# Kernel tuning notes

Hardware: AMD Instinct MI355X
Metric: run time of the kernel (lower is better)

The kernel has to match this reference:

```python
import jax, jax.numpy as jnp
import numpy as np

B, S, D_IN, D_OUT, N_EXPERTS = 8, 4096, 512, 512, 8


def setup_inputs() -> dict:
    key = jax.random.key(0)
    k1, k2, k3, k4 = jax.random.split(key, 4)
    x = jax.random.normal(k1, (B, S, D_IN), dtype=jnp.float32)
    partitions = jax.random.randint(k2, (B, S), 0, N_EXPERTS, dtype=jnp.int32)
    # per-branch nn.Linear weights: [n, out_features, in_features], kaiming-ish scale
    W = jax.random.normal(k3, (N_EXPERTS, D_OUT, D_IN), dtype=jnp.float32) * 0.03
    b = jax.random.normal(k4, (N_EXPERTS, D_OUT), dtype=jnp.float32) * 0.01
    return {"x": x, "partitions": partitions, "W": W, "b": b}


def reference(x, partitions, W, b):
    # Hard token partition -> per-branch linear -> scatter combine.
    # Equivalent math to dynamic_partition + branch Linear + dynamic_stitch:
    # out[t] = x[t] @ W[p[t]].T + b[p[t]]
    in_shape = x.shape
    xf = x.reshape(-1, in_shape[-1])          # [T, d_in]
    p = partitions.reshape(-1)                # [T]
    # Compute all-expert outputs, then select per-token expert (vectorized
    # replacement for the variable-size per-partition GEMM loop).
    y = jnp.einsum('td,eod->teo', xf, W) + b[None, :, :]   # [T, n, d_out]
    out = jnp.take_along_axis(y, p[:, None, None], axis=1)[:, 0, :]  # [T, d_out]
    return out.reshape(in_shape[:-1] + (W.shape[1],))
```

## Files before the change

### kernel.cpp

```cpp
#include <hip/hip_runtime.h>
#include <hip/hip_bf16.h>

#define N_EXPERTS 8
#define T_TOKENS 32768
#define D 512
#define TILE 128
#define BK 64
#define MAX_MTILES 264
#define SORT_CAP (MAX_MTILES * TILE)

typedef __bf16 bf16x8 __attribute__((ext_vector_type(8)));
typedef float  f32x4  __attribute__((ext_vector_type(4)));
typedef unsigned short u16x8 __attribute__((ext_vector_type(8)));

__device__ __forceinline__ unsigned short f2bf(float f) {
    unsigned int u = __float_as_uint(f);
    u += 0x7FFFu + ((u >> 16) & 1u);
    return (unsigned short)(u >> 16);
}

__device__ __forceinline__ void gl2lds16(const void* g, void* l) {
    __builtin_amdgcn_global_load_lds(
        (const __attribute__((address_space(1))) void*)g,
        (__attribute__((address_space(3))) void*)l, 16, 0, 0);
}

__global__ void hist_kernel(const int* __restrict__ p, int* __restrict__ counts) {
    __shared__ int h[N_EXPERTS];
    int tid = threadIdx.x;
    if (tid < N_EXPERTS) h[tid] = 0;
    __syncthreads();
    for (int t = blockIdx.x * blockDim.x + tid; t < T_TOKENS; t += gridDim.x * blockDim.x)
        atomicAdd(&h[p[t]], 1);
    __syncthreads();
    if (tid < N_EXPERTS) atomicAdd(&counts[tid], h[tid]);
}

__global__ void offsets_kernel(const int* __restrict__ counts, int* __restrict__ ps) {
    int acc = 0;
    for (int e = 0; e < N_EXPERTS; e++) {
        ps[e] = acc;
        acc += ((counts[e] + TILE - 1) / TILE) * TILE;
    }
    ps[N_EXPERTS] = acc;
}

__global__ void scatter_kernel(const int* __restrict__ p, const int* __restrict__ ps,
                               int* __restrict__ fill, int* __restrict__ sorted) {
    __shared__ int lcount[N_EXPERTS];
    __shared__ int lbase[N_EXPERTS];
    int tid = threadIdx.x;
    if (tid < N_EXPERTS) lcount[tid] = 0;
    __syncthreads();
    int t = blockIdx.x * blockDim.x + tid;
    int e = 0, lrank = 0;
    if (t < T_TOKENS) {
        e = p[t];
        lrank = atomicAdd(&lcount[e], 1);
    }
    __syncthreads();
    if (tid < N_EXPERTS)
        lbase[tid] = (lcount[tid] > 0) ? atomicAdd(&fill[tid], lcount[tid]) : 0;
    __syncthreads();
    if (t < T_TOKENS)
        sorted[ps[e] + lbase[e] + lrank] = t;
}

__global__ __launch_bounds__(256) void gather_convert_x(
        const float* __restrict__ x, const int* __restrict__ sorted,
        const int* __restrict__ ps, unsigned short* __restrict__ xs) {
    int row = blockIdx.x * 4 + (threadIdx.x >> 6);
    if (row >= ps[N_EXPERTS]) return;
    int lane = threadIdx.x & 63;
    int tok = sorted[row];
    u16x8 o;
    if (tok >= 0) {
        const float4* src = (const float4*)(x + (size_t)tok * D + lane * 8);
        float4 a = src[0], b = src[1];
        o[0] = f2bf(a.x); o[1] = f2bf(a.y); o[2] = f2bf(a.z); o[3] = f2bf(a.w);
        o[4] = f2bf(b.x); o[5] = f2bf(b.y); o[6] = f2bf(b.z); o[7] = f2bf(b.w);
    } else {
        o = (u16x8)0;
    }
    *(u16x8*)&xs[(size_t)row * D + lane * 8] = o;
}

__global__ __launch_bounds__(256) void convert_w(
        const float* __restrict__ W, unsigned short* __restrict__ Wb) {
    size_t i = (size_t)(blockIdx.x * 256 + threadIdx.x) * 8;
    const float4* s = (const float4*)(W + i);
    float4 a = s[0], b = s[1];
    u16x8 o;
    o[0] = f2bf(a.x); o[1] = f2bf(a.y); o[2] = f2bf(a.z); o[3] = f2bf(a.w);
    o[4] = f2bf(b.x); o[5] = f2bf(b.y); o[6] = f2bf(b.z); o[7] = f2bf(b.w);
    *(u16x8*)&Wb[i] = o;
}

__global__ __launch_bounds__(256) void moe_gemm_bf16(
        const unsigned short* __restrict__ xs, const unsigned short* __restrict__ Wb,
        const float* __restrict__ bias, const int* __restrict__ ps,
        const int* __restrict__ sorted, float* __restrict__ out) {
    __shared__ int s_idx[TILE];
    __shared__ unsigned short sA[TILE * BK];
    __shared__ unsigned short sB[TILE * BK];

    int bn = blockIdx.x, bm = blockIdx.y;
    int row0 = bm * TILE;
    int total = ps[N_EXPERTS];
    if (row0 >= total) return;
    int e = 0;
    while (row0 >= ps[e + 1]) e++;

    int tid = threadIdx.x;
    if (tid < TILE) s_idx[tid] = sorted[row0 + tid];

    int wave = tid >> 6, lane = tid & 63;
    int wm = (wave >> 1) * 64, wn = (wave & 1) * 64;
    int lrow = lane & 15, lq = lane >> 4;

    int srow = lane >> 3;
    int swz = (lane & 7) ^ srow;
    const unsigned short* gA = xs + (size_t)(row0 + wave * 32 + srow) * D + swz * 8;
    const unsigned short* gB = Wb + (size_t)e * D * D
                             + (size_t)(bn * TILE + wave * 32 + srow) * D + swz * 8;
    unsigned short* lA = sA + (wave * 32) * BK;
    unsigned short* lB = sB + (wave * 32) * BK;

    f32x4 acc[4][4];
#pragma unroll
    for (int i = 0; i < 4; i++)
#pragma unroll
        for (int j = 0; j < 4; j++)
            acc[i][j] = (f32x4){0.f, 0.f, 0.f, 0.f};

    for (int kk = 0; kk < D; kk += BK) {
        __syncthreads();
#pragma unroll
        for (int t = 0; t < 4; t++) {
            gl2lds16(gA + (size_t)(t * 8) * D + kk, lA + t * 8 * BK);
            gl2lds16(gB + (size_t)(t * 8) * D + kk, lB + t * 8 * BK);
        }
        __syncthreads();
#pragma unroll
        for (int ks = 0; ks < 2; ks++) {
            bf16x8 af[4], bfr[4];
#pragma unroll
            for (int i = 0; i < 4; i++) {
                int row = wm + 16 * i + lrow;
                int cb = (ks * 4 + lq) ^ (lrow & 7);
                af[i] = *(const bf16x8*)&sA[row * BK + cb * 8];
            }
#pragma unroll
            for (int j = 0; j < 4; j++) {
                int row = wn + 16 * j + lrow;
                int cb = (ks * 4 + lq) ^ (lrow & 7);
                bfr[j] = *(const bf16x8*)&sB[row * BK + cb * 8];
            }
#pragma unroll
            for (int i = 0; i < 4; i++)
#pragma unroll
                for (int j = 0; j < 4; j++)
                    acc[i][j] = __builtin_amdgcn_mfma_f32_16x16x32_bf16(
                        af[i], bfr[j], acc[i][j], 0, 0, 0);
        }
    }

#pragma unroll
    for (int j = 0; j < 4; j++) {
        int ng = bn * TILE + wn + 16 * j + lrow;
        float bv = bias[e * D + ng];
#pragma unroll
        for (int i = 0; i < 4; i++) {
#pragma unroll
            for (int r = 0; r < 4; r++) {
                int mrow = wm + 16 * i + lq * 4 + r;
                int tok = s_idx[mrow];
                if (tok >= 0)
                    out[(size_t)tok * D + ng] = acc[i][j][r] + bv;
            }
        }
    }
}

__global__ __launch_bounds__(256) void moe_gemm_f32(
        const float* __restrict__ x, const float* __restrict__ W,
        const float* __restrict__ bias, const int* __restrict__ ps,
        const int* __restrict__ sorted, float* __restrict__ out) {
    __shared__ int s_idx[TILE];
    __shared__ unsigned short sA[TILE][BK + 8];
    __shared__ unsigned short sB[TILE][BK + 8];

    int bm = blockIdx.x, bn = blockIdx.y;
    int row0 = bm * TILE;
    int total = ps[N_EXPERTS];
    if (row0 >= total) return;
    int e = 0;
    while (row0 >= ps[e + 1]) e++;

    int tid = threadIdx.x;
    if (tid < TILE) s_idx[tid] = sorted[row0 + tid];
    __syncthreads();

    const float* Wb = W + (size_t)e * D * D + (size_t)(bn * TILE) * D;

    f32x4 acc[4][4];
#pragma unroll
    for (int i = 0; i < 4; i++)
#pragma unroll
        for (int j = 0; j < 4; j++)
            acc[i][j] = (f32x4){0.f, 0.f, 0.f, 0.f};

    int wave = tid >> 6, lane = tid & 63;
    int wm = (wave >> 1) * 64, wn = (wave & 1) * 64;
    int lrow = lane & 15, lq = lane >> 4;

    for (int kk = 0; kk < D; kk += BK) {
#pragma unroll
        for (int i = 0; i < 8; i++) {
            int flat = tid + i * 256;
            int r = flat >> 4, c = (flat & 15) << 2;
            int tok = s_idx[r];
            float4 v = make_float4(0.f, 0.f, 0.f, 0.f);
            if (tok >= 0) v = *(const float4*)(x + (size_t)tok * D + kk + c);
            ushort4 w4;
            w4.x = f2bf(v.x); w4.y = f2bf(v.y); w4.z = f2bf(v.z); w4.w = f2bf(v.w);
            *(ushort4*)&sA[r][c] = w4;
        }
#pragma unroll
        for (int i = 0; i < 8; i++) {
            int flat = tid + i * 256;
            int r = flat >> 4, c = (flat & 15) << 2;
            float4 v = *(const float4*)(Wb + (size_t)r * D + kk + c);
            ushort4 w4;
            w4.x = f2bf(v.x); w4.y = f2bf(v.y); w4.z = f2bf(v.z); w4.w = f2bf(v.w);
            *(ushort4*)&sB[r][c] = w4;
        }
        __syncthreads();
#pragma unroll
        for (int ks = 0; ks < 2; ks++) {
            bf16x8 af[4], bfr[4];
#pragma unroll
            for (int i = 0; i < 4; i++)
                af[i] = *(const bf16x8*)&sA[wm + 16 * i + lrow][ks * 32 + lq * 8];
#pragma unroll
            for (int j = 0; j < 4; j++)
                bfr[j] = *(const bf16x8*)&sB[wn + 16 * j + lrow][ks * 32 + lq * 8];
#pragma unroll
            for (int i = 0; i < 4; i++)
#pragma unroll
                for (int j = 0; j < 4; j++)
                    acc[i][j] = __builtin_amdgcn_mfma_f32_16x16x32_bf16(
                        af[i], bfr[j], acc[i][j], 0, 0, 0);
        }
        __syncthreads();
    }

#pragma unroll
    for (int j = 0; j < 4; j++) {
        int ng = bn * TILE + wn + 16 * j + lrow;
        float bv = bias[e * D + ng];
#pragma unroll
        for (int i = 0; i < 4; i++) {
#pragma unroll
            for (int r = 0; r < 4; r++) {
                int mrow = wm + 16 * i + lq * 4 + r;
                int tok = s_idx[mrow];
                if (tok >= 0)
                    out[(size_t)tok * D + ng] = acc[i][j][r] + bv;
            }
        }
    }
}

extern "C" void kernel_launch(void* const* d_in, const int* in_sizes, int n_in,
                              void* d_out, int out_size, void* d_ws, size_t ws_size,
                              hipStream_t stream) {
    const float* x    = (const float*)d_in[0];
    const int*   part = (const int*)d_in[1];
    const float* W    = (const float*)d_in[2];
    const float* b    = (const float*)d_in[3];
    float* out = (float*)d_out;

    const size_t xs_elems = (size_t)SORT_CAP * D;
    const size_t wb_elems = (size_t)N_EXPERTS * D * D;
    const size_t fast_bytes = (xs_elems + wb_elems) * 2 + SORT_CAP * 4 + 32 * 4;

    if (ws_size >= fast_bytes) {
        unsigned short* xs = (unsigned short*)d_ws;
        unsigned short* Wb = xs + xs_elems;
        int* sorted = (int*)(Wb + wb_elems);
        int* counts = sorted + SORT_CAP;
        int* fill   = counts + N_EXPERTS;
        int* ps     = fill + N_EXPERTS;

        hipMemsetAsync(sorted, 0xFF, SORT_CAP * sizeof(int), stream);
        hipMemsetAsync(counts, 0, (2 * N_EXPERTS + N_EXPERTS + 1) * sizeof(int), stream);

        hist_kernel<<<64, 256, 0, stream>>>(part, counts);
        offsets_kernel<<<1, 1, 0, stream>>>(counts, ps);
        scatter_kernel<<<(T_TOKENS + 255) / 256, 256, 0, stream>>>(part, ps, fill, sorted);
        gather_convert_x<<<SORT_CAP / 4, 256, 0, stream>>>(x, sorted, ps, xs);
        convert_w<<<(int)(wb_elems / 8 / 256), 256, 0, stream>>>(W, Wb);

        dim3 grid(D / TILE, MAX_MTILES);
        moe_gemm_bf16<<<grid, 256, 0, stream>>>(xs, Wb, b, ps, sorted, out);
    } else {
        int* sorted = (int*)d_ws;
        int* counts = sorted + SORT_CAP;
        int* fill   = counts + N_EXPERTS;
        int* ps     = fill + N_EXPERTS;

        hipMemsetAsync(sorted, 0xFF, SORT_CAP * sizeof(int), stream);
        hipMemsetAsync(counts, 0, (2 * N_EXPERTS + N_EXPERTS + 1) * sizeof(int), stream);

        hist_kernel<<<64, 256, 0, stream>>>(part, counts);
        offsets_kernel<<<1, 1, 0, stream>>>(counts, ps);
        scatter_kernel<<<(T_TOKENS + 255) / 256, 256, 0, stream>>>(part, ps, fill, sorted);

        dim3 grid(MAX_MTILES, D / TILE);
        moe_gemm_f32<<<grid, 256, 0, stream>>>(x, W, b, ps, sorted, out);
    }
}
```

Measured before the change: 187.9 us.

## Fuse offset and convert kernels, load GEMM fragments directly from global memory

Drops the single-thread offsets kernel: scatter, convert and GEMM each recompute the padded expert prefix sums from the counts. The x-gather/convert and W-convert kernels are merged into one launch. The bf16 GEMM no longer stages tiles through LDS. Each wave loads its MFMA fragments from global memory into double-buffered registers, removing the barriers and LDS traffic but duplicating global and cache reads across waves. The prefetch on the last iteration also reads one step past the end of K.

```diff
diff --git a/kernel.cpp b/kernel.cpp
--- a/kernel.cpp
+++ b/kernel.cpp
@@ -5,9 +5,10 @@
 #define T_TOKENS 32768
 #define D 512
 #define TILE 128
-#define BK 64
 #define MAX_MTILES 264
 #define SORT_CAP (MAX_MTILES * TILE)
+#define GCX_BLOCKS (SORT_CAP / 4)
+#define WCV_BLOCKS ((N_EXPERTS * D * D) / (256 * 8))
 
 typedef __bf16 bf16x8 __attribute__((ext_vector_type(8)));
 typedef float  f32x4  __attribute__((ext_vector_type(4)));
@@ -19,11 +20,7 @@
     return (unsigned short)(u >> 16);
 }
 
-__device__ __forceinline__ void gl2lds16(const void* g, void* l) {
-    __builtin_amdgcn_global_load_lds(
-        (const __attribute__((address_space(1))) void*)g,
-        (__attribute__((address_space(3))) void*)l, 16, 0, 0);
-}
+__device__ __forceinline__ int pad_tile(int c) { return (c + TILE - 1) & ~(TILE - 1); }
 
 __global__ void hist_kernel(const int* __restrict__ p, int* __restrict__ counts) {
     __shared__ int h[N_EXPERTS];
@@ -36,16 +33,7 @@
     if (tid < N_EXPERTS) atomicAdd(&counts[tid], h[tid]);
 }
 
-__global__ void offsets_kernel(const int* __restrict__ counts, int* __restrict__ ps) {
-    int acc = 0;
-    for (int e = 0; e < N_EXPERTS; e++) {
-        ps[e] = acc;
-        acc += ((counts[e] + TILE - 1) / TILE) * TILE;
-    }
-    ps[N_EXPERTS] = acc;
-}
-
-__global__ void scatter_kernel(const int* __restrict__ p, const int* __restrict__ ps,
+__global__ void scatter_kernel(const int* __restrict__ p, const int* __restrict__ counts,
                                int* __restrict__ fill, int* __restrict__ sorted) {
     __shared__ int lcount[N_EXPERTS];
     __shared__ int lbase[N_EXPERTS];
@@ -62,69 +50,75 @@
     if (tid < N_EXPERTS)
         lbase[tid] = (lcount[tid] > 0) ? atomicAdd(&fill[tid], lcount[tid]) : 0;
     __syncthreads();
-    if (t < T_TOKENS)
-        sorted[ps[e] + lbase[e] + lrank] = t;
-}
-
-__global__ __launch_bounds__(256) void gather_convert_x(
-        const float* __restrict__ x, const int* __restrict__ sorted,
-        const int* __restrict__ ps, unsigned short* __restrict__ xs) {
-    int row = blockIdx.x * 4 + (threadIdx.x >> 6);
-    if (row >= ps[N_EXPERTS]) return;
-    int lane = threadIdx.x & 63;
-    int tok = sorted[row];
-    u16x8 o;
-    if (tok >= 0) {
-        const float4* src = (const float4*)(x + (size_t)tok * D + lane * 8);
-        float4 a = src[0], b = src[1];
+    if (t < T_TOKENS) {
+        int base = 0;
+#pragma unroll
+        for (int i = 0; i < N_EXPERTS; i++)
+            if (e > i) base += pad_tile(counts[i]);
+        sorted[base + lbase[e] + lrank] = t;
+    }
+}
+
+__global__ __launch_bounds__(256) void convert_kernel(
+        const float* __restrict__ x, const float* __restrict__ W,
+        const int* __restrict__ sorted, const int* __restrict__ counts,
+        unsigned short* __restrict__ xs, unsigned short* __restrict__ Wb) {
+    int bid = blockIdx.x;
+    if (bid < GCX_BLOCKS) {
+        int row = bid * 4 + (threadIdx.x >> 6);
+        int total = 0;
+#pragma unroll
+        for (int i = 0; i < N_EXPERTS; i++) total += pad_tile(counts[i]);
+        if (row >= total) return;
+        int lane = threadIdx.x & 63;
+        int tok = sorted[row];
+        u16x8 o;
+        if (tok >= 0) {
+            const float4* src = (const float4*)(x + (size_t)tok * D + lane * 8);
+            float4 a = src[0], b = src[1];
+            o[0] = f2bf(a.x); o[1] = f2bf(a.y); o[2] = f2bf(a.z); o[3] = f2bf(a.w);
+            o[4] = f2bf(b.x); o[5] = f2bf(b.y); o[6] = f2bf(b.z); o[7] = f2bf(b.w);
+        } else {
+            o = (u16x8)0;
+        }
+        *(u16x8*)&xs[(size_t)row * D + lane * 8] = o;
+    } else {
+        size_t i = ((size_t)(bid - GCX_BLOCKS) * 256 + threadIdx.x) * 8;
+        const float4* s = (const float4*)(W + i);
+        float4 a = s[0], b = s[1];
+        u16x8 o;
         o[0] = f2bf(a.x); o[1] = f2bf(a.y); o[2] = f2bf(a.z); o[3] = f2bf(a.w);
         o[4] = f2bf(b.x); o[5] = f2bf(b.y); o[6] = f2bf(b.z); o[7] = f2bf(b.w);
-    } else {
-        o = (u16x8)0;
-    }
-    *(u16x8*)&xs[(size_t)row * D + lane * 8] = o;
-}
-
-__global__ __launch_bounds__(256) void convert_w(
-        const float* __restrict__ W, unsigned short* __restrict__ Wb) {
-    size_t i = (size_t)(blockIdx.x * 256 + threadIdx.x) * 8;
-    const float4* s = (const float4*)(W + i);
-    float4 a = s[0], b = s[1];
-    u16x8 o;
-    o[0] = f2bf(a.x); o[1] = f2bf(a.y); o[2] = f2bf(a.z); o[3] = f2bf(a.w);
-    o[4] = f2bf(b.x); o[5] = f2bf(b.y); o[6] = f2bf(b.z); o[7] = f2bf(b.w);
-    *(u16x8*)&Wb[i] = o;
-}
-
-__global__ __launch_bounds__(256) void moe_gemm_bf16(
+        *(u16x8*)&Wb[i] = o;
+    }
+}
+
+__global__ __launch_bounds__(256) void moe_gemm_direct(
         const unsigned short* __restrict__ xs, const unsigned short* __restrict__ Wb,
-        const float* __restrict__ bias, const int* __restrict__ ps,
+        const float* __restrict__ bias, const int* __restrict__ counts,
         const int* __restrict__ sorted, float* __restrict__ out) {
     __shared__ int s_idx[TILE];
-    __shared__ unsigned short sA[TILE * BK];
-    __shared__ unsigned short sB[TILE * BK];
-
     int bn = blockIdx.x, bm = blockIdx.y;
     int row0 = bm * TILE;
-    int total = ps[N_EXPERTS];
+    int total = 0, e = 0;
+#pragma unroll
+    for (int i = 0; i < N_EXPERTS; i++) {
+        int sz = pad_tile(counts[i]);
+        if (row0 >= total + sz) e = i + 1;
+        total += sz;
+    }
     if (row0 >= total) return;
-    int e = 0;
-    while (row0 >= ps[e + 1]) e++;
 
     int tid = threadIdx.x;
     if (tid < TILE) s_idx[tid] = sorted[row0 + tid];
+    __syncthreads();
 
     int wave = tid >> 6, lane = tid & 63;
     int wm = (wave >> 1) * 64, wn = (wave & 1) * 64;
     int lrow = lane & 15, lq = lane >> 4;
 
-    int srow = lane >> 3;
-    int swz = (lane & 7) ^ srow;
-    const unsigned short* gA = xs + (size_t)(row0 + wave * 32 + srow) * D + swz * 8;
-    const unsigned short* gB = Wb + (size_t)e * D * D
-                             + (size_t)(bn * TILE + wave * 32 + srow) * D + swz * 8;
-    unsigned short* lA = sA + (wave * 32) * BK;
-    unsigned short* lB = sB + (wave * 32) * BK;
+    const unsigned short* Ap = xs + (size_t)(row0 + wm + lrow) * D + lq * 8;
+    const unsigned short* Bp = Wb + ((size_t)e * D + bn * TILE + wn + lrow) * D + lq * 8;
 
     f32x4 acc[4][4];
 #pragma unroll
@@ -133,37 +127,31 @@
         for (int j = 0; j < 4; j++)
             acc[i][j] = (f32x4){0.f, 0.f, 0.f, 0.f};
 
-    for (int kk = 0; kk < D; kk += BK) {
-        __syncthreads();
-#pragma unroll
-        for (int t = 0; t < 4; t++) {
-            gl2lds16(gA + (size_t)(t * 8) * D + kk, lA + t * 8 * BK);
-            gl2lds16(gB + (size_t)(t * 8) * D + kk, lB + t * 8 * BK);
-        }
-        __syncthreads();
-#pragma unroll
-        for (int ks = 0; ks < 2; ks++) {
-            bf16x8 af[4], bfr[4];
-#pragma unroll
-            for (int i = 0; i < 4; i++) {
-                int row = wm + 16 * i + lrow;
-                int cb = (ks * 4 + lq) ^ (lrow & 7);
-                af[i] = *(const bf16x8*)&sA[row * BK + cb * 8];
-            }
-#pragma unroll
-            for (int j = 0; j < 4; j++) {
-                int row = wn + 16 * j + lrow;
-                int cb = (ks * 4 + lq) ^ (lrow & 7);
-                bfr[j] = *(const bf16x8*)&sB[row * BK + cb * 8];
-            }
-#pragma unroll
-            for (int i = 0; i < 4; i++)
-#pragma unroll
-                for (int j = 0; j < 4; j++)
-                    acc[i][j] = __builtin_amdgcn_mfma_f32_16x16x32_bf16(
-                        af[i], bfr[j], acc[i][j], 0, 0, 0);
-        }
-    }
+    bf16x8 a0[4], b0[4], a1[4], b1[4];
+
+#define LOADF(av, bv, ks) do {                                                  \
+    _Pragma("unroll") for (int i = 0; i < 4; i++)                               \
+        av[i] = *(const bf16x8*)(Ap + i * 16 * D + (ks) * 32);                  \
+    _Pragma("unroll") for (int j = 0; j < 4; j++)                               \
+        bv[j] = *(const bf16x8*)(Bp + j * 16 * D + (ks) * 32);                  \
+} while (0)
+#define MFMAF(av, bv) do {                                                      \
+    _Pragma("unroll") for (int i = 0; i < 4; i++)                               \
+    _Pragma("unroll") for (int j = 0; j < 4; j++)                               \
+        acc[i][j] = __builtin_amdgcn_mfma_f32_16x16x32_bf16(                    \
+            av[i], bv[j], acc[i][j], 0, 0, 0);                                  \
+} while (0)
+
+    LOADF(a0, b0, 0);
+#pragma unroll 1
+    for (int ks = 0; ks < 16; ks += 2) {
+        LOADF(a1, b1, ks + 1);
+        MFMAF(a0, b0);
+        LOADF(a0, b0, ks + 2);
+        MFMAF(a1, b1);
+    }
+#undef LOADF
+#undef MFMAF
 
 #pragma unroll
     for (int j = 0; j < 4; j++) {
@@ -184,18 +172,22 @@
 
 __global__ __launch_bounds__(256) void moe_gemm_f32(
         const float* __restrict__ x, const float* __restrict__ W,
-        const float* __restrict__ bias, const int* __restrict__ ps,
+        const float* __restrict__ bias, const int* __restrict__ counts,
         const int* __restrict__ sorted, float* __restrict__ out) {
     __shared__ int s_idx[TILE];
-    __shared__ unsigned short sA[TILE][BK + 8];
-    __shared__ unsigned short sB[TILE][BK + 8];
+    __shared__ unsigned short sA[TILE][64 + 8];
+    __shared__ unsigned short sB[TILE][64 + 8];
 
     int bm = blockIdx.x, bn = blockIdx.y;
     int row0 = bm * TILE;
-    int total = ps[N_EXPERTS];
+    int total = 0, e = 0;
+#pragma unroll
+    for (int i = 0; i < N_EXPERTS; i++) {
+        int sz = pad_tile(counts[i]);
+        if (row0 >= total + sz) e = i + 1;
+        total += sz;
+    }
     if (row0 >= total) return;
-    int e = 0;
-    while (row0 >= ps[e + 1]) e++;
 
     int tid = threadIdx.x;
     if (tid < TILE) s_idx[tid] = sorted[row0 + tid];
@@ -214,7 +206,7 @@
     int wm = (wave >> 1) * 64, wn = (wave & 1) * 64;
     int lrow = lane & 15, lq = lane >> 4;
 
-    for (int kk = 0; kk < D; kk += BK) {
+    for (int kk = 0; kk < D; kk += 64) {
 #pragma unroll
         for (int i = 0; i < 8; i++) {
             int flat = tid + i * 256;
@@ -291,33 +283,28 @@
         int* sorted = (int*)(Wb + wb_elems);
         int* counts = sorted + SORT_CAP;
         int* fill   = counts + N_EXPERTS;
-        int* ps     = fill + N_EXPERTS;
 
         hipMemsetAsync(sorted, 0xFF, SORT_CAP * sizeof(int), stream);
-        hipMemsetAsync(counts, 0, (2 * N_EXPERTS + N_EXPERTS + 1) * sizeof(int), stream);
+        hipMemsetAsync(counts, 0, 2 * N_EXPERTS * sizeof(int), stream);
 
         hist_kernel<<<64, 256, 0, stream>>>(part, counts);
-        offsets_kernel<<<1, 1, 0, stream>>>(counts, ps);
-        scatter_kernel<<<(T_TOKENS + 255) / 256, 256, 0, stream>>>(part, ps, fill, sorted);
-        gather_convert_x<<<SORT_CAP / 4, 256, 0, stream>>>(x, sorted, ps, xs);
-        convert_w<<<(int)(wb_elems / 8 / 256), 256, 0, stream>>>(W, Wb);
+        scatter_kernel<<<(T_TOKENS + 255) / 256, 256, 0, stream>>>(part, counts, fill, sorted);
+        convert_kernel<<<GCX_BLOCKS + WCV_BLOCKS, 256, 0, stream>>>(x, W, sorted, counts, xs, Wb);
 
         dim3 grid(D / TILE, MAX_MTILES);
-        moe_gemm_bf16<<<grid, 256, 0, stream>>>(xs, Wb, b, ps, sorted, out);
+        moe_gemm_direct<<<grid, 256, 0, stream>>>(xs, Wb, b, counts, sorted, out);
     } else {
         int* sorted = (int*)d_ws;
         int* counts = sorted + SORT_CAP;
         int* fill   = counts + N_EXPERTS;
-        int* ps     = fill + N_EXPERTS;
 
         hipMemsetAsync(sorted, 0xFF, SORT_CAP * sizeof(int), stream);
-        hipMemsetAsync(counts, 0, (2 * N_EXPERTS + N_EXPERTS + 1) * sizeof(int), stream);
+        hipMemsetAsync(counts, 0, 2 * N_EXPERTS * sizeof(int), stream);
 
         hist_kernel<<<64, 256, 0, stream>>>(part, counts);
-        offsets_kernel<<<1, 1, 0, stream>>>(counts, ps);
-        scatter_kernel<<<(T_TOKENS + 255) / 256, 256, 0, stream>>>(part, ps, fill, sorted);
+        scatter_kernel<<<(T_TOKENS + 255) / 256, 256, 0, stream>>>(part, counts, fill, sorted);
 
         dim3 grid(MAX_MTILES, D / TILE);
-        moe_gemm_f32<<<grid, 256, 0, stream>>>(x, W, b, ps, sorted, out);
-    }
-}
+        moe_gemm_f32<<<grid, 256, 0, stream>>>(x, W, b, counts, sorted, out);
+    }
+}
```

Measured after the change: 231.2 us. 23.0% more time.
